# Performance work log

Measured on AMD Instinct MI355X. Metric: run time of the kernel, lower is better.

## Reference

```python
import jax, jax.numpy as jnp
import numpy as np

EMBED_DIM = 1024
NUM_HEADS = 16
HEAD_DIM = EMBED_DIM // NUM_HEADS
THETA = 10000.0


def setup_inputs() -> dict:
    key = jax.random.key(0)
    ks = jax.random.split(key, 5)
    B, S, E = 2, 2048, EMBED_DIM
    x = jax.random.normal(ks[0], (B, S, E), dtype=jnp.float32)
    s = 1.0 / np.sqrt(E)
    Wq = jax.random.normal(ks[1], (E, E), dtype=jnp.float32) * s
    Wk = jax.random.normal(ks[2], (E, E), dtype=jnp.float32) * s
    Wv = jax.random.normal(ks[3], (E, E), dtype=jnp.float32) * s
    Wo = jax.random.normal(ks[4], (E, E), dtype=jnp.float32) * s
    bo = jnp.zeros((E,), dtype=jnp.float32)
    return {"x": x, "Wq": Wq, "Wk": Wk, "Wv": Wv, "Wo": Wo, "bo": bo}


def _apply_rope(t, cos, sin):
    # t: (B, H, S, D); cos, sin: (S, D/2)
    t1 = t[..., 0::2]
    t2 = t[..., 1::2]
    r1 = t1 * cos - t2 * sin
    r2 = t1 * sin + t2 * cos
    # interleave back: (..., D/2, 2) -> (..., D)
    return jnp.stack([r1, r2], axis=-1).reshape(t.shape)


def reference(x, Wq, Wk, Wv, Wo, bo):
    B, S, E = x.shape
    H, D = NUM_HEADS, HEAD_DIM
    scale = D ** -0.5

    # projections (torch Linear: y = x @ W.T)
    q = (x @ Wq.T).reshape(B, S, H, D).transpose(0, 2, 1, 3)
    k = (x @ Wk.T).reshape(B, S, H, D).transpose(0, 2, 1, 3)
    v = (x @ Wv.T).reshape(B, S, H, D).transpose(0, 2, 1, 3)

    # fixed RoPE freqs (temporal, non-learned)
    freqs = 1.0 / THETA ** (jnp.arange(0, D, 2, dtype=jnp.float32) / D)  # (D/2,)
    pos = jnp.arange(S, dtype=jnp.float32)
    angles = pos[:, None] * freqs[None, :]  # (S, D/2)
    cos, sin = jnp.cos(angles), jnp.sin(angles)

    q = _apply_rope(q, cos, sin)
    k = _apply_rope(k, cos, sin)

    attn = jnp.einsum('bhqd,bhkd->bhqk', q, k) * scale
    attn = jax.nn.softmax(attn, axis=-1)
    out = jnp.einsum('bhqk,bhkd->bhqd', attn, v)
    out = out.transpose(0, 2, 1, 3).reshape(B, S, E)
    return out @ Wo.T + bo
```

## Files before the change

kernel.cpp:

```cpp
#include <hip/hip_runtime.h>


typedef __attribute__((ext_vector_type(8))) short bf16x8;
typedef __attribute__((ext_vector_type(4))) float f32x4;
typedef unsigned short u16;
typedef unsigned int u32;

#define MFMA(a, b, c) __builtin_amdgcn_mfma_f32_16x16x32_bf16((a), (b), (c), 0, 0, 0)

#define GLOAD16(g, l)                                                        \
  __builtin_amdgcn_global_load_lds((const __attribute__((address_space(1))) void*)(g), \
                                   (__attribute__((address_space(3))) void*)(l), 16, 0, 0)

__device__ __forceinline__ float bf2f(u16 u) {
  union { u32 i; float f; } v; v.i = ((u32)u) << 16; return v.f;
}
__device__ __forceinline__ u16 f2bf(float f) {
  union { float f; u32 i; } v; v.f = f;
  u32 x = v.i;
  return (u16)((x + 0x7fffu + ((x >> 16) & 1u)) >> 16);
}

__global__ __launch_bounds__(256) void cast_kernel(const float* __restrict__ in,
                                                   u16* __restrict__ out, int n8) {
  int i = blockIdx.x * 256 + threadIdx.x;
  if (i >= n8) return;
  const float4* p = (const float4*)in + 2 * (size_t)i;
  float4 a = p[0], b = p[1];
  bf16x8 o;
  o[0] = (short)f2bf(a.x); o[1] = (short)f2bf(a.y);
  o[2] = (short)f2bf(a.z); o[3] = (short)f2bf(a.w);
  o[4] = (short)f2bf(b.x); o[5] = (short)f2bf(b.y);
  o[6] = (short)f2bf(b.z); o[7] = (short)f2bf(b.w);
  *(bf16x8*)(out + 8 * (size_t)i) = o;
}

__global__ __launch_bounds__(256) void cast4_kernel(const float* __restrict__ a,
                                                    const float* __restrict__ b,
                                                    const float* __restrict__ c,
                                                    const float* __restrict__ d,
                                                    u16* __restrict__ oa, u16* __restrict__ ob,
                                                    u16* __restrict__ oc, u16* __restrict__ od) {
  int i = blockIdx.x * 256 + threadIdx.x;
  int sel = i >> 17, r = i & 131071;
  const float* src = sel == 0 ? a : sel == 1 ? b : sel == 2 ? c : d;
  u16* dst = sel == 0 ? oa : sel == 1 ? ob : sel == 2 ? oc : od;
  const float4* p = (const float4*)src + 2 * (size_t)r;
  float4 x = p[0], y = p[1];
  bf16x8 o;
  o[0] = (short)f2bf(x.x); o[1] = (short)f2bf(x.y);
  o[2] = (short)f2bf(x.z); o[3] = (short)f2bf(x.w);
  o[4] = (short)f2bf(y.x); o[5] = (short)f2bf(y.y);
  o[6] = (short)f2bf(y.z); o[7] = (short)f2bf(y.w);
  *(bf16x8*)(dst + 8 * (size_t)r) = o;
}

__global__ __launch_bounds__(256) void rope_table_kernel(float* __restrict__ cosT,
                                                         float* __restrict__ sinT) {
  int i = blockIdx.x * 256 + threadIdx.x;
  int s = i >> 5, p = i & 31;
  float freq = powf(10000.0f, -(float)(2 * p) / 64.0f);
  float ang = (float)s * freq;
  cosT[i] = cosf(ang);
  sinT[i] = sinf(ang);
}

template <bool FINAL>
__global__ __launch_bounds__(256) void gemm_bt_kernel(
    const u16* __restrict__ A, const u16* __restrict__ B0, const u16* __restrict__ B1,
    const u16* __restrict__ B2, u16* __restrict__ Cb, float* __restrict__ Cf,
    const float* __restrict__ bias, int Ntot) {
  const int K = 1024;
  const int tid = threadIdx.x, lane = tid & 63, wid = tid >> 6;
  const int wr = wid >> 1, wc = wid & 1;
  const int m0 = blockIdx.y * 128;
  const int nt = blockIdx.x;
  const int n0 = nt * 128;
  const u16* Bt;
  int nloc0;
  if (!FINAL) {
    int sel = nt >> 3;
    Bt = sel == 0 ? B0 : (sel == 1 ? B1 : B2);
    nloc0 = n0 & 1023;
  } else {
    Bt = B0;
    nloc0 = n0;
  }

  __shared__ u16 As[128 * 64];
  __shared__ u16 Bs[128 * 64];

  f32x4 acc[4][4];
#pragma unroll
  for (int i = 0; i < 4; i++)
#pragma unroll
    for (int j = 0; j < 4; j++) acc[i][j] = f32x4{0.f, 0.f, 0.f, 0.f};

  const int strow = tid >> 3;
  const int sgcol0 = (tid & 7) * 8;

  auto stage = [&](int k0) {
#pragma unroll
    for (int p = 0; p < 4; ++p) {
      int row = p * 32 + strow;
      int gcol = sgcol0 ^ ((row & 7) << 3);
      const u16* ga = A + (size_t)(m0 + row) * K + k0 + gcol;
      const u16* gb = Bt + (size_t)(nloc0 + row) * K + k0 + gcol;
      u16* la = As + (p * 256 + wid * 64) * 8;
      u16* lb = Bs + (p * 256 + wid * 64) * 8;
      GLOAD16(ga, la);
      GLOAD16(gb, lb);
    }
  };

  for (int k0 = 0; k0 < K; k0 += 64) {
    stage(k0);
    __syncthreads();
#pragma unroll
    for (int kk = 0; kk < 2; ++kk) {
      bf16x8 af[4], bfr[4];
#pragma unroll
      for (int i = 0; i < 4; ++i) {
        int row = wr * 64 + i * 16 + (lane & 15);
        int col = (kk * 32 + (lane >> 4) * 8) ^ ((row & 7) << 3);
        af[i] = *(const bf16x8*)(As + row * 64 + col);
      }
#pragma unroll
      for (int j = 0; j < 4; ++j) {
        int row = wc * 64 + j * 16 + (lane & 15);
        int col = (kk * 32 + (lane >> 4) * 8) ^ ((row & 7) << 3);
        bfr[j] = *(const bf16x8*)(Bs + row * 64 + col);
      }
#pragma unroll
      for (int i = 0; i < 4; ++i)
#pragma unroll
        for (int j = 0; j < 4; ++j) acc[i][j] = MFMA(af[i], bfr[j], acc[i][j]);
    }
    __syncthreads();
  }

#pragma unroll
  for (int i = 0; i < 4; ++i)
#pragma unroll
    for (int j = 0; j < 4; ++j)
#pragma unroll
      for (int r = 0; r < 4; ++r) {
        int row = m0 + wr * 64 + i * 16 + (lane >> 4) * 4 + r;
        int col = n0 + wc * 64 + j * 16 + (lane & 15);
        if (FINAL)
          Cf[(size_t)row * Ntot + col] = acc[i][j][r] + bias[col];
        else
          Cb[(size_t)row * Ntot + col] = f2bf(acc[i][j][r]);
      }
}

__global__ __launch_bounds__(256) void rope_apply_kernel(
    const u16* __restrict__ C, const float* __restrict__ cosT, const float* __restrict__ sinT,
    u16* __restrict__ Qo, u16* __restrict__ Ko) {
  int idx = blockIdx.x * 256 + threadIdx.x;
  int p = idx & 31, h = (idx >> 5) & 15, m = idx >> 9;
  int s = m & 2047, b = m >> 11;
  float c = cosT[s * 32 + p], sn = sinT[s * 32 + p];
  size_t src = (size_t)m * 3072 + h * 64 + 2 * p;
  u32 qu = *(const u32*)(C + src);
  u32 ku = *(const u32*)(C + src + 1024);
  float q0 = bf2f((u16)qu), q1 = bf2f((u16)(qu >> 16));
  float k0 = bf2f((u16)ku), k1 = bf2f((u16)(ku >> 16));
  float qr0 = (q0 * c - q1 * sn) * 0.125f;
  float qr1 = (q0 * sn + q1 * c) * 0.125f;
  float kr0 = k0 * c - k1 * sn;
  float kr1 = k0 * sn + k1 * c;
  size_t dst = ((size_t)(b * 16 + h) * 2048 + s) * 64 + 2 * p;
  *(u32*)(Qo + dst) = (u32)f2bf(qr0) | ((u32)f2bf(qr1) << 16);
  *(u32*)(Ko + dst) = (u32)f2bf(kr0) | ((u32)f2bf(kr1) << 16);
}

__global__ __launch_bounds__(256) void transpose_v_kernel(const u16* __restrict__ C,
                                                          u16* __restrict__ VT) {
  int st = blockIdx.x, bh = blockIdx.y;
  int b = bh >> 4, h = bh & 15;
  __shared__ u16 tile[64][72];
  int t = threadIdx.x;
#pragma unroll
  for (int p = 0; p < 2; ++p) {
    int r = p * 32 + (t >> 3), cb = (t & 7) * 8;
    bf16x8 v = *(const bf16x8*)(C + (size_t)(b * 2048 + st * 64 + r) * 3072 + 2048 + h * 64 + cb);
    *(bf16x8*)(&tile[r][cb]) = v;
  }
  __syncthreads();
#pragma unroll
  for (int p = 0; p < 2; ++p) {
    int d = p * 32 + (t >> 3), sb = (t & 7) * 8;
    bf16x8 v;
#pragma unroll
    for (int j = 0; j < 8; ++j) v[j] = (short)tile[sb + j][d];
    *(bf16x8*)(VT + ((size_t)bh * 64 + d) * 2048 + st * 64 + sb) = v;
  }
}

__global__ __launch_bounds__(256) void attn_kernel(
    const u16* __restrict__ Q, const u16* __restrict__ Kk, const u16* __restrict__ VT,
    u16* __restrict__ O) {
  const int qt = blockIdx.x, bh = blockIdx.y;
  const int tid = threadIdx.x, lane = tid & 63, wid = tid >> 6;
  const int b = bh >> 4, h = bh & 15;

  __shared__ u16 Ks[2][64 * 64];
  __shared__ u16 Vs[2][64 * 64];
  __shared__ u16 Ps[4][16 * 64];

  const int qrow = qt * 64 + wid * 16 + (lane & 15);
  const size_t qbase = ((size_t)bh * 2048 + qrow) * 64;
  bf16x8 qf[2];
  qf[0] = *(const bf16x8*)(Q + qbase + (lane >> 4) * 8);
  qf[1] = *(const bf16x8*)(Q + qbase + 32 + (lane >> 4) * 8);

  f32x4 o[4];
#pragma unroll
  for (int j = 0; j < 4; ++j) o[j] = f32x4{0.f, 0.f, 0.f, 0.f};
  float lsum[4] = {0.f, 0.f, 0.f, 0.f};

  const u16* Kb = Kk + (size_t)bh * 2048 * 64;
  const u16* Vb = VT + (size_t)bh * 64 * 2048;

  const int strow = tid >> 3;
  const int sgc0 = (tid & 7) * 8;
  auto stage = [&](int t, int buf) {
#pragma unroll
    for (int p = 0; p < 2; ++p) {
      int row = p * 32 + strow;
      int gcol = sgc0 ^ ((row & 7) << 3);
      const u16* gk = Kb + (size_t)(t * 64 + row) * 64 + gcol;
      const u16* gv = Vb + (size_t)row * 2048 + t * 64 + gcol;
      u16* lk = Ks[buf] + (p * 256 + wid * 64) * 8;
      u16* lv = Vs[buf] + (p * 256 + wid * 64) * 8;
      GLOAD16(gk, lk);
      GLOAD16(gv, lv);
    }
  };

  stage(0, 0);
  char* Pw = (char*)&Ps[wid][0];
  for (int t = 0; t < 32; ++t) {
    const int buf = t & 1;
    __syncthreads();
    if (t + 1 < 32) stage(t + 1, buf ^ 1);

    f32x4 sc4[4];
#pragma unroll
    for (int j = 0; j < 4; ++j) sc4[j] = f32x4{0.f, 0.f, 0.f, 0.f};
#pragma unroll
    for (int kk = 0; kk < 2; ++kk) {
      bf16x8 kf[4];
#pragma unroll
      for (int j = 0; j < 4; ++j) {
        int row = j * 16 + (lane & 15);
        int col = (kk * 32 + (lane >> 4) * 8) ^ ((row & 7) << 3);
        kf[j] = *(const bf16x8*)(Ks[buf] + row * 64 + col);
      }
#pragma unroll
      for (int j = 0; j < 4; ++j) sc4[j] = MFMA(qf[kk], kf[j], sc4[j]);
    }

#pragma unroll
    for (int j = 0; j < 4; ++j)
#pragma unroll
      for (int r = 0; r < 4; ++r) {
        float pv = __expf(sc4[j][r] - 24.0f);
        lsum[r] += pv;
        int prow = (lane >> 4) * 4 + r, pcol = j * 16 + (lane & 15);
        int off = (prow * 128 + pcol * 2) ^ ((prow & 7) << 4);
        *(u16*)(Pw + off) = f2bf(pv);
      }

#pragma unroll
    for (int kk = 0; kk < 2; ++kk) {
      int prow = lane & 15;
      int poff = (prow * 128 + kk * 64 + (lane >> 4) * 16) ^ ((prow & 7) << 4);
      bf16x8 pf = *(const bf16x8*)(Pw + poff);
      bf16x8 vf[4];
#pragma unroll
      for (int j = 0; j < 4; ++j) {
        int vrow = j * 16 + (lane & 15);
        int vcol = (kk * 32 + (lane >> 4) * 8) ^ ((vrow & 7) << 3);
        vf[j] = *(const bf16x8*)(Vs[buf] + vrow * 64 + vcol);
      }
#pragma unroll
      for (int j = 0; j < 4; ++j) o[j] = MFMA(pf, vf[j], o[j]);
    }
  }

#pragma unroll
  for (int r = 0; r < 4; ++r) {
#pragma unroll
    for (int d = 1; d < 16; d <<= 1) lsum[r] += __shfl_xor(lsum[r], d, 64);
  }

#pragma unroll
  for (int j = 0; j < 4; ++j)
#pragma unroll
    for (int r = 0; r < 4; ++r) {
      int srow = qt * 64 + wid * 16 + (lane >> 4) * 4 + r;
      int col = h * 64 + j * 16 + (lane & 15);
      float val = o[j][r] * __frcp_rn(lsum[r]);
      O[(size_t)(b * 2048 + srow) * 1024 + col] = f2bf(val);
    }
}

extern "C" void kernel_launch(void* const* d_in, const int* in_sizes, int n_in,
                              void* d_out, int out_size, void* d_ws, size_t ws_size,
                              hipStream_t stream) {
  const float* x = (const float*)d_in[0];
  const float* Wq = (const float*)d_in[1];
  const float* Wk = (const float*)d_in[2];
  const float* Wv = (const float*)d_in[3];
  const float* Wo = (const float*)d_in[4];
  const float* bo = (const float*)d_in[5];

  char* ws = (char*)d_ws;
  size_t off = 0;
  auto carve = [&](size_t bytes) {
    void* pp = ws + off;
    off += (bytes + 255) & ~(size_t)255;
    return pp;
  };
  u16* xb = (u16*)carve(4194304ull * 2);
  u16* Wqb = (u16*)carve(1048576ull * 2);
  u16* Wkb = (u16*)carve(1048576ull * 2);
  u16* Wvb = (u16*)carve(1048576ull * 2);
  u16* Wob = (u16*)carve(1048576ull * 2);
  float* cosT = (float*)carve(65536ull * 4);
  float* sinT = (float*)carve(65536ull * 4);
  u16* Cqkv = (u16*)carve(4096ull * 3072 * 2);
  u16* q_r = (u16*)carve(4194304ull * 2);
  u16* k_r = (u16*)carve(4194304ull * 2);
  u16* vT = (u16*)carve(4194304ull * 2);
  u16* attn_out = Cqkv;

  cast_kernel<<<2048, 256, 0, stream>>>(x, xb, 524288);
  cast4_kernel<<<2048, 256, 0, stream>>>(Wq, Wk, Wv, Wo, Wqb, Wkb, Wvb, Wob);
  rope_table_kernel<<<256, 256, 0, stream>>>(cosT, sinT);

  gemm_bt_kernel<false><<<dim3(24, 32), 256, 0, stream>>>(xb, Wqb, Wkb, Wvb, Cqkv, nullptr,
                                                          nullptr, 3072);
  rope_apply_kernel<<<8192, 256, 0, stream>>>(Cqkv, cosT, sinT, q_r, k_r);
  transpose_v_kernel<<<dim3(32, 32), 256, 0, stream>>>(Cqkv, vT);
  attn_kernel<<<dim3(32, 32), 256, 0, stream>>>(q_r, k_r, vT, attn_out);
  gemm_bt_kernel<true><<<dim3(8, 32), 256, 0, stream>>>(attn_out, Wob, nullptr, nullptr, nullptr,
                                                        (float*)d_out, bo, 1024);
}
```

Measured before the change: 221.8 us.

## Fuse RoPE and V transpose into QKV GEMM epilogue; merge prep kernels

The three cast and RoPE-table kernels are merged into one prep launch. The QKV GEMM epilogue now applies RoPE and the query scale directly, pairing even and odd columns with a lane shuffle, and writes V transposed, so the intermediate QKV buffer and two separate passes over it are no longer needed. In attention, the bf16 conversion of P becomes truncation, and the row sum uses the same truncated value. The cost is scattered epilogue stores (strided ushort4 writes for V^T) and slightly different rounding from truncating P.

```diff
diff --git a/kernel.cpp b/kernel.cpp
--- a/kernel.cpp
+++ b/kernel.cpp
@@ -21,55 +21,49 @@
   return (u16)((x + 0x7fffu + ((x >> 16) & 1u)) >> 16);
 }
 
-__global__ __launch_bounds__(256) void cast_kernel(const float* __restrict__ in,
-                                                   u16* __restrict__ out, int n8) {
-  int i = blockIdx.x * 256 + threadIdx.x;
-  if (i >= n8) return;
-  const float4* p = (const float4*)in + 2 * (size_t)i;
-  float4 a = p[0], b = p[1];
-  bf16x8 o;
-  o[0] = (short)f2bf(a.x); o[1] = (short)f2bf(a.y);
-  o[2] = (short)f2bf(a.z); o[3] = (short)f2bf(a.w);
-  o[4] = (short)f2bf(b.x); o[5] = (short)f2bf(b.y);
-  o[6] = (short)f2bf(b.z); o[7] = (short)f2bf(b.w);
-  *(bf16x8*)(out + 8 * (size_t)i) = o;
-}
-
-__global__ __launch_bounds__(256) void cast4_kernel(const float* __restrict__ a,
-                                                    const float* __restrict__ b,
-                                                    const float* __restrict__ c,
-                                                    const float* __restrict__ d,
-                                                    u16* __restrict__ oa, u16* __restrict__ ob,
-                                                    u16* __restrict__ oc, u16* __restrict__ od) {
-  int i = blockIdx.x * 256 + threadIdx.x;
-  int sel = i >> 17, r = i & 131071;
-  const float* src = sel == 0 ? a : sel == 1 ? b : sel == 2 ? c : d;
-  u16* dst = sel == 0 ? oa : sel == 1 ? ob : sel == 2 ? oc : od;
-  const float4* p = (const float4*)src + 2 * (size_t)r;
-  float4 x = p[0], y = p[1];
-  bf16x8 o;
-  o[0] = (short)f2bf(x.x); o[1] = (short)f2bf(x.y);
-  o[2] = (short)f2bf(x.z); o[3] = (short)f2bf(x.w);
-  o[4] = (short)f2bf(y.x); o[5] = (short)f2bf(y.y);
-  o[6] = (short)f2bf(y.z); o[7] = (short)f2bf(y.w);
-  *(bf16x8*)(dst + 8 * (size_t)r) = o;
-}
-
-__global__ __launch_bounds__(256) void rope_table_kernel(float* __restrict__ cosT,
-                                                         float* __restrict__ sinT) {
-  int i = blockIdx.x * 256 + threadIdx.x;
-  int s = i >> 5, p = i & 31;
-  float freq = powf(10000.0f, -(float)(2 * p) / 64.0f);
-  float ang = (float)s * freq;
-  cosT[i] = cosf(ang);
-  sinT[i] = sinf(ang);
-}
-
-template <bool FINAL>
+__global__ __launch_bounds__(256) void prep_kernel(
+    const float* __restrict__ x, const float* __restrict__ Wq, const float* __restrict__ Wk,
+    const float* __restrict__ Wv, const float* __restrict__ Wo, u16* __restrict__ xb,
+    u16* __restrict__ Wqb, u16* __restrict__ Wkb, u16* __restrict__ Wvb, u16* __restrict__ Wob,
+    float* __restrict__ cosT, float* __restrict__ sinT) {
+  int bid = blockIdx.x;
+  if (bid < 4096) {
+    int i = bid * 256 + threadIdx.x;
+    const float* src;
+    u16* dst;
+    int r;
+    if (i < 524288) {
+      src = x; dst = xb; r = i;
+    } else {
+      int k = i - 524288, sel = k >> 17;
+      r = k & 131071;
+      src = sel == 0 ? Wq : sel == 1 ? Wk : sel == 2 ? Wv : Wo;
+      dst = sel == 0 ? Wqb : sel == 1 ? Wkb : sel == 2 ? Wvb : Wob;
+    }
+    const float4* p = (const float4*)src + 2 * (size_t)r;
+    float4 a = p[0], b = p[1];
+    bf16x8 o;
+    o[0] = (short)f2bf(a.x); o[1] = (short)f2bf(a.y);
+    o[2] = (short)f2bf(a.z); o[3] = (short)f2bf(a.w);
+    o[4] = (short)f2bf(b.x); o[5] = (short)f2bf(b.y);
+    o[6] = (short)f2bf(b.z); o[7] = (short)f2bf(b.w);
+    *(bf16x8*)(dst + 8 * (size_t)r) = o;
+  } else {
+    int i = (bid - 4096) * 256 + threadIdx.x;
+    int s = i >> 5, p = i & 31;
+    float freq = powf(10000.0f, -(float)(2 * p) / 64.0f);
+    float ang = (float)s * freq;
+    cosT[i] = cosf(ang);
+    sinT[i] = sinf(ang);
+  }
+}
+
+template <int MODE>
 __global__ __launch_bounds__(256) void gemm_bt_kernel(
     const u16* __restrict__ A, const u16* __restrict__ B0, const u16* __restrict__ B1,
-    const u16* __restrict__ B2, u16* __restrict__ Cb, float* __restrict__ Cf,
-    const float* __restrict__ bias, int Ntot) {
+    const u16* __restrict__ B2, u16* __restrict__ Qo, u16* __restrict__ Ko,
+    u16* __restrict__ VT, const float* __restrict__ cosT, const float* __restrict__ sinT,
+    float* __restrict__ Cf, const float* __restrict__ bias, int Ntot) {
   const int K = 1024;
   const int tid = threadIdx.x, lane = tid & 63, wid = tid >> 6;
   const int wr = wid >> 1, wc = wid & 1;
@@ -77,12 +71,13 @@
   const int nt = blockIdx.x;
   const int n0 = nt * 128;
   const u16* Bt;
-  int nloc0;
-  if (!FINAL) {
-    int sel = nt >> 3;
+  int nloc0, sel;
+  if (MODE == 0) {
+    sel = nt >> 3;
     Bt = sel == 0 ? B0 : (sel == 1 ? B1 : B2);
     nloc0 = n0 & 1023;
   } else {
+    sel = 0;
     Bt = B0;
     nloc0 = n0;
   }
@@ -139,62 +134,67 @@
     __syncthreads();
   }
 
-#pragma unroll
-  for (int i = 0; i < 4; ++i)
-#pragma unroll
-    for (int j = 0; j < 4; ++j)
-#pragma unroll
-      for (int r = 0; r < 4; ++r) {
-        int row = m0 + wr * 64 + i * 16 + (lane >> 4) * 4 + r;
-        int col = n0 + wc * 64 + j * 16 + (lane & 15);
-        if (FINAL)
+  if (MODE == 1) {
+#pragma unroll
+    for (int i = 0; i < 4; ++i)
+#pragma unroll
+      for (int j = 0; j < 4; ++j)
+#pragma unroll
+        for (int r = 0; r < 4; ++r) {
+          int row = m0 + wr * 64 + i * 16 + (lane >> 4) * 4 + r;
+          int col = n0 + wc * 64 + j * 16 + (lane & 15);
           Cf[(size_t)row * Ntot + col] = acc[i][j][r] + bias[col];
-        else
-          Cb[(size_t)row * Ntot + col] = f2bf(acc[i][j][r]);
-      }
-}
-
-__global__ __launch_bounds__(256) void rope_apply_kernel(
-    const u16* __restrict__ C, const float* __restrict__ cosT, const float* __restrict__ sinT,
-    u16* __restrict__ Qo, u16* __restrict__ Ko) {
-  int idx = blockIdx.x * 256 + threadIdx.x;
-  int p = idx & 31, h = (idx >> 5) & 15, m = idx >> 9;
-  int s = m & 2047, b = m >> 11;
-  float c = cosT[s * 32 + p], sn = sinT[s * 32 + p];
-  size_t src = (size_t)m * 3072 + h * 64 + 2 * p;
-  u32 qu = *(const u32*)(C + src);
-  u32 ku = *(const u32*)(C + src + 1024);
-  float q0 = bf2f((u16)qu), q1 = bf2f((u16)(qu >> 16));
-  float k0 = bf2f((u16)ku), k1 = bf2f((u16)(ku >> 16));
-  float qr0 = (q0 * c - q1 * sn) * 0.125f;
-  float qr1 = (q0 * sn + q1 * c) * 0.125f;
-  float kr0 = k0 * c - k1 * sn;
-  float kr1 = k0 * sn + k1 * c;
-  size_t dst = ((size_t)(b * 16 + h) * 2048 + s) * 64 + 2 * p;
-  *(u32*)(Qo + dst) = (u32)f2bf(qr0) | ((u32)f2bf(qr1) << 16);
-  *(u32*)(Ko + dst) = (u32)f2bf(kr0) | ((u32)f2bf(kr1) << 16);
-}
-
-__global__ __launch_bounds__(256) void transpose_v_kernel(const u16* __restrict__ C,
-                                                          u16* __restrict__ VT) {
-  int st = blockIdx.x, bh = blockIdx.y;
-  int b = bh >> 4, h = bh & 15;
-  __shared__ u16 tile[64][72];
-  int t = threadIdx.x;
-#pragma unroll
-  for (int p = 0; p < 2; ++p) {
-    int r = p * 32 + (t >> 3), cb = (t & 7) * 8;
-    bf16x8 v = *(const bf16x8*)(C + (size_t)(b * 2048 + st * 64 + r) * 3072 + 2048 + h * 64 + cb);
-    *(bf16x8*)(&tile[r][cb]) = v;
-  }
-  __syncthreads();
-#pragma unroll
-  for (int p = 0; p < 2; ++p) {
-    int d = p * 32 + (t >> 3), sb = (t & 7) * 8;
-    bf16x8 v;
-#pragma unroll
-    for (int j = 0; j < 8; ++j) v[j] = (short)tile[sb + j][d];
-    *(bf16x8*)(VT + ((size_t)bh * 64 + d) * 2048 + st * 64 + sb) = v;
+        }
+    return;
+  }
+
+  const int par = lane & 1;
+  if (sel < 2) {
+    u16* dst = sel == 0 ? Qo : Ko;
+    const float mul = sel == 0 ? 0.125f : 1.0f;
+#pragma unroll
+    for (int i = 0; i < 4; ++i) {
+      int rowb = m0 + wr * 64 + i * 16 + (lane >> 4) * 4;
+      int s = rowb & 2047, b = rowb >> 11;
+#pragma unroll
+      for (int j = 0; j < 4; ++j) {
+        int col = nloc0 + wc * 64 + j * 16 + (lane & 15);
+        int h = col >> 6, dd = col & 63, p = dd >> 1;
+        size_t base = ((size_t)(b * 16 + h) * 2048 + s) * 64 + (dd & ~1);
+#pragma unroll
+        for (int r = 0; r < 4; ++r) {
+          float v = acc[i][j][r];
+          float other = __shfl_xor(v, 1, 64);
+          float t1 = par ? other : v;
+          float t2 = par ? v : other;
+          float c = cosT[(s + r) * 32 + p];
+          float sn = sinT[(s + r) * 32 + p];
+          float r0 = (t1 * c - t2 * sn) * mul;
+          float r1 = (t1 * sn + t2 * c) * mul;
+          if (!par) {
+            u32 pk = (u32)f2bf(r0) | ((u32)f2bf(r1) << 16);
+            *(u32*)(dst + base + (size_t)r * 64) = pk;
+          }
+        }
+      }
+    }
+  } else {
+#pragma unroll
+    for (int i = 0; i < 4; ++i) {
+      int rowb = m0 + wr * 64 + i * 16 + (lane >> 4) * 4;
+      int s = rowb & 2047, b = rowb >> 11;
+#pragma unroll
+      for (int j = 0; j < 4; ++j) {
+        int col = nloc0 + wc * 64 + j * 16 + (lane & 15);
+        int h = col >> 6, dd = col & 63;
+        ushort4 pk;
+        pk.x = f2bf(acc[i][j][0]);
+        pk.y = f2bf(acc[i][j][1]);
+        pk.z = f2bf(acc[i][j][2]);
+        pk.w = f2bf(acc[i][j][3]);
+        *(ushort4*)(VT + ((size_t)(b * 16 + h) * 64 + dd) * 2048 + s) = pk;
+      }
+    }
   }
 }
 
@@ -267,10 +267,14 @@
 #pragma unroll
       for (int r = 0; r < 4; ++r) {
         float pv = __expf(sc4[j][r] - 24.0f);
-        lsum[r] += pv;
+        union { float f; u32 i; } uu;
+        uu.f = pv;
+        u32 bits = uu.i;
+        uu.i = bits & 0xffff0000u;
+        lsum[r] += uu.f;
         int prow = (lane >> 4) * 4 + r, pcol = j * 16 + (lane & 15);
         int off = (prow * 128 + pcol * 2) ^ ((prow & 7) << 4);
-        *(u16*)(Pw + off) = f2bf(pv);
+        *(u16*)(Pw + off) = (u16)(bits >> 16);
       }
 
 #pragma unroll
@@ -331,21 +335,16 @@
   u16* Wob = (u16*)carve(1048576ull * 2);
   float* cosT = (float*)carve(65536ull * 4);
   float* sinT = (float*)carve(65536ull * 4);
-  u16* Cqkv = (u16*)carve(4096ull * 3072 * 2);
   u16* q_r = (u16*)carve(4194304ull * 2);
   u16* k_r = (u16*)carve(4194304ull * 2);
   u16* vT = (u16*)carve(4194304ull * 2);
-  u16* attn_out = Cqkv;
-
-  cast_kernel<<<2048, 256, 0, stream>>>(x, xb, 524288);
-  cast4_kernel<<<2048, 256, 0, stream>>>(Wq, Wk, Wv, Wo, Wqb, Wkb, Wvb, Wob);
-  rope_table_kernel<<<256, 256, 0, stream>>>(cosT, sinT);
-
-  gemm_bt_kernel<false><<<dim3(24, 32), 256, 0, stream>>>(xb, Wqb, Wkb, Wvb, Cqkv, nullptr,
-                                                          nullptr, 3072);
-  rope_apply_kernel<<<8192, 256, 0, stream>>>(Cqkv, cosT, sinT, q_r, k_r);
-  transpose_v_kernel<<<dim3(32, 32), 256, 0, stream>>>(Cqkv, vT);
+  u16* attn_out = (u16*)carve(4194304ull * 2);
+
+  prep_kernel<<<4352, 256, 0, stream>>>(x, Wq, Wk, Wv, Wo, xb, Wqb, Wkb, Wvb, Wob, cosT, sinT);
+  gemm_bt_kernel<0><<<dim3(24, 32), 256, 0, stream>>>(xb, Wqb, Wkb, Wvb, q_r, k_r, vT, cosT,
+                                                      sinT, nullptr, nullptr, 3072);
   attn_kernel<<<dim3(32, 32), 256, 0, stream>>>(q_r, k_r, vT, attn_out);
-  gemm_bt_kernel<true><<<dim3(8, 32), 256, 0, stream>>>(attn_out, Wob, nullptr, nullptr, nullptr,
-                                                        (float*)d_out, bo, 1024);
-}
+  gemm_bt_kernel<1><<<dim3(8, 32), 256, 0, stream>>>(attn_out, Wob, nullptr, nullptr, nullptr,
+                                                     nullptr, nullptr, nullptr, nullptr,
+                                                     (float*)d_out, bo, 1024);
+}
```

After: 231.7 us. 1.04x slower.
